# Optimization experiments

Measured on AMD Instinct MI355X. Metric: run time of the kernel, lower is better.

The kernel has to match this reference:

```python
import jax, jax.numpy as jnp
import numpy as np

L_LAYERS = 3
HIDDEN = 768
HEADS = 8
K_NEIGH = 5
LN_EPS = 1e-5


def layer_norm(x, scale, bias):
    mu = x.mean(-1, keepdims=True)
    var = ((x - mu) ** 2).mean(-1, keepdims=True)
    return (x - mu) * jax.lax.rsqrt(var + LN_EPS) * scale + bias


def build_adj_norm(x):
    """Dynamic kNN graph (topk on x x^T, symmetrized, dedup via boolean adjacency)
    with GCN self-loops and symmetric D^-1/2 A D^-1/2 normalization."""
    B, S, _ = x.shape
    sim = jnp.einsum('bsd,btd->bst', x, x)                     # [B,S,S]
    _, idx = jax.lax.top_k(sim, K_NEIGH)                        # [B,S,k]
    adj = jnp.zeros((B, S, S), dtype=bool)
    adj = adj.at[jnp.arange(B)[:, None, None],
                 jnp.arange(S)[None, :, None], idx].set(True)
    adj = adj | adj.transpose(0, 2, 1)                          # symmetrize (unique implied)
    adj = adj | jnp.eye(S, dtype=bool)[None]                    # remaining self-loops
    A = adj.astype(x.dtype)
    dinv = jax.lax.rsqrt(A.sum(-1))                             # deg>=1 always
    return dinv[:, :, None] * A * dinv[:, None, :]


def mha(x, w_in, b_in, w_out, b_out):
    B, S, D = x.shape
    d = D // HEADS
    qkv = x @ w_in + b_in                                       # [B,S,3D]
    q, k, v = jnp.split(qkv, 3, axis=-1)
    q = q.reshape(B, S, HEADS, d).transpose(0, 2, 1, 3)
    k = k.reshape(B, S, HEADS, d).transpose(0, 2, 1, 3)
    v = v.reshape(B, S, HEADS, d).transpose(0, 2, 1, 3)
    scores = jnp.einsum('bhqd,bhkd->bhqk', q, k) * (1.0 / np.sqrt(d))
    attn = jax.nn.softmax(scores, axis=-1)
    o = jnp.einsum('bhqk,bhkd->bhqd', attn, v)
    o = o.transpose(0, 2, 1, 3).reshape(B, S, D)
    return o @ w_out + b_out


def setup_inputs() -> dict:
    key = jax.random.key(0)
    ks = jax.random.split(key, 16)
    D, L = HIDDEN, L_LAYERS
    s = 0.02
    inp = {
        'x': jax.random.normal(ks[0], (8, 1024, D), dtype=jnp.float32),
        'gcn_w': jax.random.normal(ks[1], (L, D, D), dtype=jnp.float32) * s,
        'gcn_b': jnp.zeros((L, D), dtype=jnp.float32),
        'attn_in_w': jax.random.normal(ks[2], (L, D, 3 * D), dtype=jnp.float32) * s,
        'attn_in_b': jnp.zeros((L, 3 * D), dtype=jnp.float32),
        'attn_out_w': jax.random.normal(ks[3], (L, D, D), dtype=jnp.float32) * s,
        'attn_out_b': jnp.zeros((L, D), dtype=jnp.float32),
        'gate_w': jax.random.normal(ks[4], (L, 2 * D, D), dtype=jnp.float32) * s,
        'gate_b': jnp.zeros((L, D), dtype=jnp.float32),
        'ln_scale': jnp.ones((L, D), dtype=jnp.float32),
        'ln_bias': jnp.zeros((L, D), dtype=jnp.float32),
        'proj_w': jax.random.normal(ks[5], (D, D), dtype=jnp.float32) * s,
        'proj_b': jnp.zeros((D,), dtype=jnp.float32),
    }
    return inp


def reference(x, gcn_w, gcn_b, attn_in_w, attn_in_b, attn_out_w, attn_out_b,
              gate_w, gate_b, ln_scale, ln_bias, proj_w, proj_b):
    # Graph built once from the input embeddings (as in GCNTransformer.forward).
    A_norm = build_adj_norm(x)                                  # [B,S,S]
    h = x
    for l in range(L_LAYERS):
        gcn_out = jnp.einsum('bst,btd->bsd', A_norm, h @ gcn_w[l]) + gcn_b[l]
        attn_out = mha(h, attn_in_w[l], attn_in_b[l], attn_out_w[l], attn_out_b[l])
        gate = jax.nn.sigmoid(
            jnp.concatenate([gcn_out, attn_out], axis=-1) @ gate_w[l] + gate_b[l])
        fused = gate * gcn_out + (1.0 - gate) * attn_out
        h = layer_norm(fused + h, ln_scale[l], ln_bias[l])
    return h @ proj_w + proj_b
```

## Files before the change

kernel.cpp:

```cpp
#include <hip/hip_runtime.h>
#include <hip/hip_bf16.h>
#include <math.h>

using bf16 = __hip_bfloat16;
typedef short s16x8 __attribute__((ext_vector_type(8)));
typedef float f32x4 __attribute__((ext_vector_type(4)));

#define ROWS 8192
#define DH 768

static inline int cdiv(int a, int b) { return (a + b - 1) / b; }

__device__ __forceinline__ void gld16(const bf16* g, bf16* l)
{
    __builtin_amdgcn_global_load_lds(
        (const __attribute__((address_space(1))) void*)g,
        (__attribute__((address_space(3))) void*)l, 16, 0, 0);
}

__global__ __launch_bounds__(256)
void gemm_bf16_nt(const bf16* __restrict__ A, const bf16* __restrict__ Bt,
                  void* __restrict__ Cout, const float* __restrict__ bias,
                  int K, int lda, int ldb, int ldc,
                  long long aO, long long aI, long long bO, long long bI,
                  long long cO, long long cI, int zInner,
                  float scale, int storeBf16, int nMask)
{
    int z = blockIdx.z;
    int zo = z / zInner, zi = z - zo * zInner;
    const bf16* Ab = A + (long long)zo * aO + (long long)zi * aI;
    const bf16* Bb = Bt + (long long)zo * bO + (long long)zi * bI;
    long long cOff = (long long)zo * cO + (long long)zi * cI;

    __shared__ bf16 As[2 * 128 * 32];
    __shared__ bf16 Bs[2 * 128 * 32];

    int tid = threadIdx.x;
    int lane = tid & 63;
    int wid = tid >> 6;
    int wm = wid >> 1, wn = wid & 1;

    int nx = gridDim.x, ny = gridDim.y;
    int bx, by;
    if ((nx & 7) == 0) {
        int lin = blockIdx.y * nx + blockIdx.x;
        int t = lin >> 3;
        bx = (lin & 7) + (t / ny) * 8;
        by = t - (t / ny) * ny;
    } else { bx = blockIdx.x; by = blockIdx.y; }
    int m0 = bx * 128;
    int n0 = by * 128;

    f32x4 acc[4][4];
    f32x4 zero = {0.f, 0.f, 0.f, 0.f};
#pragma unroll
    for (int i = 0; i < 4; i++)
#pragma unroll
        for (int j = 0; j < 4; j++) acc[i][j] = zero;

    int f0 = tid, f1 = tid + 256;
    int r0 = f0 >> 2, c0 = (f0 & 3) * 8;
    int r1 = f1 >> 2, c1 = (f1 & 3) * 8;
    const bf16* a0p = Ab + (long long)(m0 + r0) * lda + c0;
    const bf16* a1p = Ab + (long long)(m0 + r1) * lda + c1;
    const bf16* b0p = Bb + (long long)(n0 + r0) * ldb + c0;
    const bf16* b1p = Bb + (long long)(n0 + r1) * ldb + c1;

    bf16* asw0 = As + wid * 512;
    bf16* asw1 = As + 2048 + wid * 512;
    bf16* bsw0 = Bs + wid * 512;
    bf16* bsw1 = Bs + 2048 + wid * 512;

    int mrow = lane & 15;
    int kcol = (lane >> 4) * 8;
    const bf16* aRead = As + (wm * 64 + mrow) * 32 + kcol;
    const bf16* bRead = Bs + (wn * 64 + mrow) * 32 + kcol;

    int nIter = K >> 5;
    gld16(a0p, asw0);
    gld16(a1p, asw1);
    gld16(b0p, bsw0);
    gld16(b1p, bsw1);

    for (int it = 0; it < nIter; it++) {
        __syncthreads();
        int cur = (it & 1) * 4096;
        int nxt = 4096 - cur;
        if (it + 1 < nIter) {
            int kn = (it + 1) << 5;
            gld16(a0p + kn, asw0 + nxt);
            gld16(a1p + kn, asw1 + nxt);
            gld16(b0p + kn, bsw0 + nxt);
            gld16(b1p + kn, bsw1 + nxt);
        }
        s16x8 af[4], bfr[4];
#pragma unroll
        for (int i = 0; i < 4; i++) af[i] = *(const s16x8*)(aRead + cur + i * 16 * 32);
#pragma unroll
        for (int i = 0; i < 4; i++) bfr[i] = *(const s16x8*)(bRead + cur + i * 16 * 32);
#pragma unroll
        for (int mi = 0; mi < 4; mi++)
#pragma unroll
            for (int ni = 0; ni < 4; ni++)
                acc[mi][ni] = __builtin_amdgcn_mfma_f32_16x16x32_bf16(
                    af[mi], bfr[ni], acc[mi][ni], 0, 0, 0);
    }

    int colL = lane & 15;
    int rq = (lane >> 4) * 4;
#pragma unroll
    for (int ni = 0; ni < 4; ni++) {
        int col = n0 + wn * 64 + ni * 16 + colL;
        if (col >= nMask) continue;
        float bv = bias ? bias[col] : 0.f;
#pragma unroll
        for (int mi = 0; mi < 4; mi++) {
#pragma unroll
            for (int r = 0; r < 4; r++) {
                int row = m0 + wm * 64 + mi * 16 + rq + r;
                float v = acc[mi][ni][r] * scale + bv;
                long long ci = cOff + (long long)row * ldc + col;
                if (storeBf16) ((bf16*)Cout)[ci] = __float2bfloat16(v);
                else           ((float*)Cout)[ci] = v;
            }
        }
    }
}

__global__ __launch_bounds__(256)
void flash_attn(const bf16* __restrict__ qkvb, const bf16* __restrict__ Vt,
                bf16* __restrict__ ob, float sscale)
{
    int qt = blockIdx.x, bh = blockIdx.y;
    int b = bh >> 3, h = bh & 7;
    int q0 = qt * 128;

    __shared__ bf16 Ks[128 * 96];
    __shared__ bf16 Ps[4 * 32 * 136];

    int tid = threadIdx.x, lane = tid & 63, wid = tid >> 6;
    int quad = lane >> 4, m16 = lane & 15;

    s16x8 qf[2][3];
#pragma unroll
    for (int s = 0; s < 2; s++) {
        int qrow = q0 + wid * 32 + s * 16 + m16;
        const bf16* qp = qkvb + (long long)(b * 1024 + qrow) * 2304 + h * 96 + quad * 8;
#pragma unroll
        for (int kk = 0; kk < 3; kk++)
            qf[s][kk] = *(const s16x8*)(qp + kk * 32);
    }

    f32x4 zero = {0.f, 0.f, 0.f, 0.f};
    f32x4 o_acc[2][6];
#pragma unroll
    for (int s = 0; s < 2; s++)
#pragma unroll
        for (int d = 0; d < 6; d++) o_acc[s][d] = zero;
    f32x4 m_run[2], l_run[2];
#pragma unroll
    for (int s = 0; s < 2; s++) {
        m_run[s] = {-3.0e38f, -3.0e38f, -3.0e38f, -3.0e38f};
        l_run[s] = zero;
    }

    bf16* Pw = Ps + wid * (32 * 136);
    const bf16* Kbase = qkvb + (long long)b * 1024 * 2304 + 768 + h * 96;
    const bf16* Vbase = Vt + (long long)bh * 128 * 1024;

    for (int kt = 0; kt < 8; kt++) {
        __syncthreads();
#pragma unroll
        for (int i = 0; i < 6; i++) {
            int gby = i * 4096 + wid * 1024 + lane * 16;
            int krow = gby / 192;
            int kcol = (gby - krow * 192) >> 1;
            gld16(Kbase + (long long)(kt * 128 + krow) * 2304 + kcol,
                  Ks + i * 2048 + wid * 512);
        }
        __syncthreads();

        f32x4 sacc[2][8];
#pragma unroll
        for (int s = 0; s < 2; s++)
#pragma unroll
            for (int j = 0; j < 8; j++) sacc[s][j] = zero;
#pragma unroll
        for (int j = 0; j < 8; j++) {
            s16x8 kf[3];
#pragma unroll
            for (int kk = 0; kk < 3; kk++)
                kf[kk] = *(const s16x8*)(Ks + (j * 16 + m16) * 96 + kk * 32 + quad * 8);
#pragma unroll
            for (int s = 0; s < 2; s++)
#pragma unroll
                for (int kk = 0; kk < 3; kk++)
                    sacc[s][j] = __builtin_amdgcn_mfma_f32_16x16x32_bf16(
                        qf[s][kk], kf[kk], sacc[s][j], 0, 0, 0);
        }

#pragma unroll
        for (int s = 0; s < 2; s++) {
#pragma unroll
            for (int j = 0; j < 8; j++)
#pragma unroll
                for (int c = 0; c < 4; c++) sacc[s][j][c] *= sscale;
            f32x4 tmax = sacc[s][0];
#pragma unroll
            for (int j = 1; j < 8; j++)
#pragma unroll
                for (int c = 0; c < 4; c++) tmax[c] = fmaxf(tmax[c], sacc[s][j][c]);
#pragma unroll
            for (int o = 1; o < 16; o <<= 1)
#pragma unroll
                for (int c = 0; c < 4; c++)
                    tmax[c] = fmaxf(tmax[c], __shfl_xor(tmax[c], o));
            f32x4 mnew, alpha;
#pragma unroll
            for (int c = 0; c < 4; c++) {
                mnew[c] = fmaxf(m_run[s][c], tmax[c]);
                alpha[c] = __expf(m_run[s][c] - mnew[c]);
            }
            f32x4 tsum = zero;
#pragma unroll
            for (int j = 0; j < 8; j++) {
#pragma unroll
                for (int c = 0; c < 4; c++) {
                    float pv = __expf(sacc[s][j][c] - mnew[c]);
                    tsum[c] += pv;
                    Pw[(s * 16 + quad * 4 + c) * 136 + j * 16 + m16] = __float2bfloat16(pv);
                }
            }
#pragma unroll
            for (int o = 1; o < 16; o <<= 1)
#pragma unroll
                for (int c = 0; c < 4; c++) tsum[c] += __shfl_xor(tsum[c], o);
#pragma unroll
            for (int c = 0; c < 4; c++)
                l_run[s][c] = l_run[s][c] * alpha[c] + tsum[c];
            m_run[s] = mnew;
#pragma unroll
            for (int d = 0; d < 6; d++)
#pragma unroll
                for (int c = 0; c < 4; c++) o_acc[s][d][c] *= alpha[c];
        }

        s16x8 pf[2][4];
#pragma unroll
        for (int s = 0; s < 2; s++)
#pragma unroll
            for (int kk = 0; kk < 4; kk++)
                pf[s][kk] = *(const s16x8*)(Pw + (s * 16 + m16) * 136 + kk * 32 + quad * 8);
#pragma unroll
        for (int dt = 0; dt < 6; dt++) {
            s16x8 vf[4];
#pragma unroll
            for (int kk = 0; kk < 4; kk++)
                vf[kk] = *(const s16x8*)(Vbase + (long long)(dt * 16 + m16) * 1024
                                         + kt * 128 + kk * 32 + quad * 8);
#pragma unroll
            for (int s = 0; s < 2; s++)
#pragma unroll
                for (int kk = 0; kk < 4; kk++)
                    o_acc[s][dt] = __builtin_amdgcn_mfma_f32_16x16x32_bf16(
                        pf[s][kk], vf[kk], o_acc[s][dt], 0, 0, 0);
        }
    }

#pragma unroll
    for (int s = 0; s < 2; s++) {
        f32x4 inv;
#pragma unroll
        for (int c = 0; c < 4; c++) inv[c] = 1.f / l_run[s][c];
#pragma unroll
        for (int dt = 0; dt < 6; dt++) {
#pragma unroll
            for (int c = 0; c < 4; c++) {
                int row = q0 + wid * 32 + s * 16 + quad * 4 + c;
                int col = h * 96 + dt * 16 + m16;
                ob[(long long)(b * 1024 + row) * 768 + col] =
                    __float2bfloat16(o_acc[s][dt][c] * inv[c]);
            }
        }
    }
}

__global__ __launch_bounds__(256)
void transpose_cast(const float* __restrict__ in, bf16* __restrict__ out, int K, int N)
{
    long long zoff = (long long)blockIdx.z * K * N;
    int k0 = blockIdx.x * 32, n0 = blockIdx.y * 32;
    __shared__ float t[32][33];
    int tx = threadIdx.x & 31, ty = threadIdx.x >> 5;
#pragma unroll
    for (int j = 0; j < 32; j += 8)
        t[ty + j][tx] = in[zoff + (long long)(k0 + ty + j) * N + n0 + tx];
    __syncthreads();
#pragma unroll
    for (int j = 0; j < 32; j += 8)
        out[zoff + (long long)(n0 + ty + j) * K + k0 + tx] = __float2bfloat16(t[tx][ty + j]);
}

__global__ void zero_u64(unsigned long long* __restrict__ p, int n)
{
    int i = blockIdx.x * 256 + threadIdx.x;
    if (i < n) p[i] = 0ull;
}

__global__ __launch_bounds__(256)
void prep_x(const float* __restrict__ x, float* __restrict__ h,
            bf16* __restrict__ hb, bf16* __restrict__ xc)
{
    int i = blockIdx.x * 256 + threadIdx.x;
    if (i >= ROWS * DH) return;
    float v = x[i];
    h[i] = v;
    bf16 h1 = __float2bfloat16(v);
    float r1 = v - __bfloat162float(h1);
    bf16 h2 = __float2bfloat16(r1);
    hb[i] = h1;
    int row = i / DH, d = i - row * DH;
    long long xb = (long long)row * 3072;
    xc[xb + d] = h1;
    xc[xb + 768 + d] = h1;
    xc[xb + 1536 + d] = h2;
    xc[xb + 2304 + d] = h1;
}

__global__ __launch_bounds__(256)
void topk_rerank(const float* __restrict__ sim, const float* __restrict__ x,
                 unsigned long long* __restrict__ mask)
{
    int row = blockIdx.x;
    int b = row >> 10, s = row & 1023;
    int tid = threadIdx.x;
    int wid = tid >> 6, lane = tid & 63;

    __shared__ float wvals[4][8];
    __shared__ int   widx[4][8];
    __shared__ int   cand[8];
    __shared__ double val[8];

    int base = wid * 256 + lane * 4;
    float4 vv = *(const float4*)(sim + (long long)row * 1024 + base);
    float v0 = vv.x, v1 = vv.y, v2 = vv.z, v3 = vv.w;

    for (int r = 0; r < 8; r++) {
        float bv = v0; int bi = base;
        if (v1 > bv) { bv = v1; bi = base + 1; }
        if (v2 > bv) { bv = v2; bi = base + 2; }
        if (v3 > bv) { bv = v3; bi = base + 3; }
#pragma unroll
        for (int o = 1; o < 64; o <<= 1) {
            float ov = __shfl_xor(bv, o);
            int   oi = __shfl_xor(bi, o);
            if (ov > bv || (ov == bv && oi < bi)) { bv = ov; bi = oi; }
        }
        if ((bi >> 2) == (wid * 64 + lane)) {
            int sl = bi & 3;
            if (sl == 0) v0 = -3.4e38f;
            else if (sl == 1) v1 = -3.4e38f;
            else if (sl == 2) v2 = -3.4e38f;
            else v3 = -3.4e38f;
        }
        if (lane == 0) { wvals[wid][r] = bv; widx[wid][r] = bi; }
    }
    __syncthreads();
    if (wid == 0) {
        float mv = -3.4e38f; int mi = 0x7fffffff;
        if (lane < 32) { mv = wvals[lane >> 3][lane & 7]; mi = widx[lane >> 3][lane & 7]; }
        for (int r = 0; r < 8; r++) {
            float bv = mv; int bi = mi;
#pragma unroll
            for (int o = 1; o < 32; o <<= 1) {
                float ov = __shfl_xor(bv, o, 32);
                int   oi = __shfl_xor(bi, o, 32);
                if (ov > bv || (ov == bv && oi < bi)) { bv = ov; bi = oi; }
            }
            if (lane < 32 && bi == mi) mv = -3.4e38f;
            if (lane == 0) cand[r] = bi;
        }
    }
    __syncthreads();
    int g = tid >> 5, t = tid & 31;
    int c = cand[g];
    const float4* xs4 = (const float4*)(x + (long long)row * DH);
    const float4* xc4 = (const float4*)(x + ((long long)b * 1024 + c) * DH);
    double acc = 0.0;
#pragma unroll
    for (int j = 0; j < 6; j++) {
        float4 a = xs4[t + j * 32];
        float4 q = xc4[t + j * 32];
        acc += (double)a.x * q.x + (double)a.y * q.y
             + (double)a.z * q.z + (double)a.w * q.w;
    }
#pragma unroll
    for (int o = 16; o; o >>= 1) acc += __shfl_xor(acc, o, 32);
    if (t == 0) val[g] = acc;
    __syncthreads();
    if (tid == 0) {
        bool used[8] = {false, false, false, false, false, false, false, false};
        for (int r = 0; r < 5; r++) {
            int best = -1;
            for (int j = 0; j < 8; j++) {
                if (used[j]) continue;
                if (best < 0 || val[j] > val[best] ||
                    (val[j] == val[best] && cand[j] < cand[best])) best = j;
            }
            used[best] = true;
            int ci = cand[best];
            atomicOr(&mask[((long long)b * 1024 + s) * 16 + (ci >> 6)], 1ull << (ci & 63));
            atomicOr(&mask[((long long)b * 1024 + ci) * 16 + (s >> 6)], 1ull << (s & 63));
        }
        atomicOr(&mask[(long long)row * 16 + (s >> 6)], 1ull << (s & 63));
    }
}

__global__ void calc_dinv(const unsigned long long* __restrict__ mask,
                          float* __restrict__ dinv, int n)
{
    int i = blockIdx.x * 256 + threadIdx.x;
    if (i >= n) return;
    int c = 0;
#pragma unroll
    for (int w = 0; w < 16; w++) c += __popcll(mask[(long long)i * 16 + w]);
    dinv[i] = 1.f / sqrtf((float)c);
}

__global__ __launch_bounds__(256)
void spmm(const unsigned long long* __restrict__ mask, const float* __restrict__ dinv,
          const float* __restrict__ g, const float* __restrict__ bias,
          float* __restrict__ out)
{
    int s = blockIdx.x, b = blockIdx.y;
    int row = b * 1024 + s;
    __shared__ unsigned long long mrow[16];
    int tid = threadIdx.x;
    if (tid < 16) mrow[tid] = mask[(long long)row * 16 + tid];
    __syncthreads();
    float ds = dinv[row];
    float a0 = 0.f, a1 = 0.f, a2 = 0.f;
    const float* gb = g + (long long)b * 1024 * DH;
    const float* db = dinv + b * 1024;
    for (int w = 0; w < 16; w++) {
        unsigned long long bits = mrow[w];
        while (bits) {
            int t = (w << 6) + __ffsll(bits) - 1;
            bits &= bits - 1;
            float c = ds * db[t];
            const float* gr = gb + (long long)t * DH;
            a0 += c * gr[tid];
            a1 += c * gr[tid + 256];
            a2 += c * gr[tid + 512];
        }
    }
    float* o = out + (long long)row * DH;
    o[tid] = a0 + bias[tid];
    o[tid + 256] = a1 + bias[tid + 256];
    o[tid + 512] = a2 + bias[tid + 512];
}

__global__ __launch_bounds__(256)
void vt_transpose(const bf16* __restrict__ qkvb, bf16* __restrict__ Vt)
{
    int bh = blockIdx.y;
    int b = bh >> 3, h = bh & 7;
    int t0 = blockIdx.x * 64;
    __shared__ bf16 tile[64][100];
    int tid = threadIdx.x;
    {
        int t = tid >> 2, c0 = (tid & 3) * 24;
        const bf16* src = qkvb + ((long long)(b * 1024 + t0 + t)) * 2304 + 1536 + h * 96 + c0;
#pragma unroll
        for (int j = 0; j < 24; j++) tile[t][c0 + j] = src[j];
    }
    __syncthreads();
    bf16* dst = Vt + ((long long)bh * 128) * 1024 + t0;
    bf16 zb = __float2bfloat16(0.f);
#pragma unroll
    for (int j = 0; j < 32; j++) {
        int f = tid + j * 256;
        int d = f >> 6, t = f & 63;
        dst[(long long)d * 1024 + t] = (d < 96) ? tile[t][d] : zb;
    }
}

__global__ void concat_cast(const float* __restrict__ gcn_out, const float* __restrict__ attn_out,
                            bf16* __restrict__ gi)
{
    int i = blockIdx.x * 256 + threadIdx.x;
    if (i >= ROWS * DH) return;
    int r = i / DH, d = i - r * DH;
    gi[(long long)r * 1536 + d] = __float2bfloat16(gcn_out[i]);
    gi[(long long)r * 1536 + 768 + d] = __float2bfloat16(attn_out[i]);
}

__global__ __launch_bounds__(256)
void fuse_ln(const float* __restrict__ gate_lin, const float* __restrict__ gcn_out,
             const float* __restrict__ attn_out, float* __restrict__ h, bf16* __restrict__ hb,
             const float* __restrict__ lns, const float* __restrict__ lnb)
{
    int row = blockIdx.x;
    long long base = (long long)row * DH;
    int tid = threadIdx.x;
    __shared__ float red[4];
    float xv[3];
#pragma unroll
    for (int j = 0; j < 3; j++) {
        int d = tid + j * 256;
        float gl = gate_lin[base + d];
        float gv = 1.f / (1.f + __expf(-gl));
        float f = gv * gcn_out[base + d] + (1.f - gv) * attn_out[base + d];
        xv[j] = f + h[base + d];
    }
    float s = xv[0] + xv[1] + xv[2];
    for (int o = 32; o; o >>= 1) s += __shfl_xor(s, o);
    if ((tid & 63) == 0) red[tid >> 6] = s;
    __syncthreads();
    float mu = (red[0] + red[1] + red[2] + red[3]) * (1.f / 768.f);
    __syncthreads();
    float vs = 0.f;
#pragma unroll
    for (int j = 0; j < 3; j++) { float c = xv[j] - mu; vs += c * c; }
    for (int o = 32; o; o >>= 1) vs += __shfl_xor(vs, o);
    if ((tid & 63) == 0) red[tid >> 6] = vs;
    __syncthreads();
    float var = (red[0] + red[1] + red[2] + red[3]) * (1.f / 768.f);
    float rs = 1.f / sqrtf(var + 1e-5f);
#pragma unroll
    for (int j = 0; j < 3; j++) {
        int d = tid + j * 256;
        float y = (xv[j] - mu) * rs * lns[d] + lnb[d];
        h[base + d] = y;
        hb[base + d] = __float2bfloat16(y);
    }
}

static void gemm(hipStream_t st, const bf16* A, const bf16* Bt, void* C, const float* bias,
                 int M, int N, int K, int lda, int ldb, int ldc,
                 long long aO, long long aI, long long bO, long long bI,
                 long long cO, long long cI, int zInner, int Z,
                 float scale, int storeBf16, int nMask)
{
    dim3 g(M / 128, (N + 127) / 128, Z);
    gemm_bf16_nt<<<g, dim3(256), 0, st>>>(A, Bt, C, bias, K, lda, ldb, ldc,
                                          aO, aI, bO, bI, cO, cI, zInner,
                                          scale, storeBf16, nMask);
}

extern "C" void kernel_launch(void* const* d_in, const int* in_sizes, int n_in,
                              void* d_out, int out_size, void* d_ws, size_t ws_size,
                              hipStream_t stream)
{
    (void)in_sizes; (void)n_in; (void)out_size; (void)ws_size;
    const float* x      = (const float*)d_in[0];
    const float* gcn_w  = (const float*)d_in[1];
    const float* gcn_b  = (const float*)d_in[2];
    const float* ain_w  = (const float*)d_in[3];
    const float* ain_b  = (const float*)d_in[4];
    const float* aout_w = (const float*)d_in[5];
    const float* aout_b = (const float*)d_in[6];
    const float* gate_w = (const float*)d_in[7];
    const float* gate_b = (const float*)d_in[8];
    const float* ln_s   = (const float*)d_in[9];
    const float* ln_b   = (const float*)d_in[10];
    const float* proj_w = (const float*)d_in[11];
    const float* proj_b = (const float*)d_in[12];
    float* out = (float*)d_out;

    char* p = (char*)d_ws;
    auto alloc = [&](size_t bytes) {
        char* r = p;
        p += (bytes + 255) & ~(size_t)255;
        return r;
    };
    bf16* gcn_wt  = (bf16*)alloc((size_t)3 * 768 * 768 * 2);
    bf16* ain_wt  = (bf16*)alloc((size_t)3 * 2304 * 768 * 2);
    bf16* aout_wt = (bf16*)alloc((size_t)3 * 768 * 768 * 2);
    bf16* gate_wt = (bf16*)alloc((size_t)3 * 768 * 1536 * 2);
    bf16* proj_wt = (bf16*)alloc((size_t)768 * 768 * 2);
    bf16* hb      = (bf16*)alloc((size_t)ROWS * DH * 2);
    float* h      = (float*)alloc((size_t)ROWS * DH * 4);
    bf16* qkvb    = (bf16*)alloc((size_t)ROWS * 2304 * 2);
    bf16* gateinb = qkvb;
    float* sim    = (float*)alloc((size_t)ROWS * 1024 * 4);
    float* attn_o = sim;
    unsigned long long* mask = (unsigned long long*)alloc((size_t)ROWS * 16 * 8);
    float* dinv   = (float*)alloc((size_t)ROWS * 4);
    float* g      = (float*)alloc((size_t)ROWS * DH * 4);
    float* gate_l = g;
    float* gcn_o  = (float*)alloc((size_t)ROWS * DH * 4);
    bf16* Vt      = (bf16*)alloc((size_t)64 * 128 * 1024 * 2);
    bf16* ob      = (bf16*)alloc((size_t)ROWS * DH * 2);
    bf16* xc      = (bf16*)g;

    transpose_cast<<<dim3(24, 24, 3), 256, 0, stream>>>(gcn_w, gcn_wt, 768, 768);
    transpose_cast<<<dim3(24, 72, 3), 256, 0, stream>>>(ain_w, ain_wt, 768, 2304);
    transpose_cast<<<dim3(24, 24, 3), 256, 0, stream>>>(aout_w, aout_wt, 768, 768);
    transpose_cast<<<dim3(48, 24, 3), 256, 0, stream>>>(gate_w, gate_wt, 1536, 768);
    transpose_cast<<<dim3(24, 24, 1), 256, 0, stream>>>(proj_w, proj_wt, 768, 768);

    prep_x<<<cdiv(ROWS * DH, 256), 256, 0, stream>>>(x, h, hb, xc);

    gemm(stream, xc, xc + 768, sim, nullptr, 1024, 1024, 2304, 3072, 3072, 1024,
         (long long)1024 * 3072, 0, (long long)1024 * 3072, 0,
         (long long)1024 * 1024, 0, 1, 8, 1.f, 0, 1024);

    zero_u64<<<cdiv(ROWS * 16, 256), 256, 0, stream>>>(mask, ROWS * 16);
    topk_rerank<<<ROWS, 256, 0, stream>>>(sim, x, mask);
    calc_dinv<<<cdiv(ROWS, 256), 256, 0, stream>>>(mask, dinv, ROWS);

    float sscale = 1.0f / sqrtf(96.0f);

    for (int l = 0; l < 3; l++) {
        gemm(stream, hb, gcn_wt + (long long)l * 768 * 768, g, nullptr,
             ROWS, 768, 768, 768, 768, 768, 0, 0, 0, 0, 0, 0, 1, 1, 1.f, 0, 768);
        spmm<<<dim3(1024, 8), 256, 0, stream>>>(mask, dinv, g, gcn_b + l * 768, gcn_o);
        gemm(stream, hb, ain_wt + (long long)l * 2304 * 768, qkvb, ain_b + l * 2304,
             ROWS, 2304, 768, 768, 768, 2304, 0, 0, 0, 0, 0, 0, 1, 1, 1.f, 1, 2304);
        vt_transpose<<<dim3(16, 64), 256, 0, stream>>>(qkvb, Vt);
        flash_attn<<<dim3(8, 64), 256, 0, stream>>>(qkvb, Vt, ob, sscale);
        gemm(stream, ob, aout_wt + (long long)l * 768 * 768, attn_o, aout_b + l * 768,
             ROWS, 768, 768, 768, 768, 768, 0, 0, 0, 0, 0, 0, 1, 1, 1.f, 0, 768);
        concat_cast<<<cdiv(ROWS * DH, 256), 256, 0, stream>>>(gcn_o, attn_o, gateinb);
        gemm(stream, gateinb, gate_wt + (long long)l * 768 * 1536, gate_l, gate_b + l * 768,
             ROWS, 768, 1536, 1536, 1536, 768, 0, 0, 0, 0, 0, 0, 1, 1, 1.f, 0, 768);
        fuse_ln<<<ROWS, 256, 0, stream>>>(gate_l, gcn_o, attn_o, h, hb,
                                          ln_s + l * 768, ln_b + l * 768);
    }

    gemm(stream, hb, proj_wt, out, proj_b,
         ROWS, 768, 768, 768, 768, 768, 0, 0, 0, 0, 0, 0, 1, 1, 1.f, 0, 768);
}
```

Before: 1.166 ms.

## Fuse GCN and QKV projections, write bf16 gate input directly, simplify sim GEMM

Concatenates the GCN weight into the QKV projection so one GEMM with N=3072 produces q, k, v and the GCN features in bf16. The spmm and output-projection GEMM now write bf16 straight into the gate-input buffer, which removes concat_cast and the fp32 intermediates. The similarity GEMM drops the split-bf16 compensated K=2304 trick and runs plain bf16 with K=768. Flash attention switches to exp2 with a log2e-folded scale and a swapped grid order. Lower precision for the GCN features and the similarity scores could change top-k neighbour selection and overall accuracy.

```diff
diff --git a/kernel.cpp b/kernel.cpp
--- a/kernel.cpp
+++ b/kernel.cpp
@@ -24,7 +24,7 @@
                   int K, int lda, int ldb, int ldc,
                   long long aO, long long aI, long long bO, long long bI,
                   long long cO, long long cI, int zInner,
-                  float scale, int storeBf16, int nMask)
+                  float scale, int storeBf16, int nMask, int biasN)
 {
     int z = blockIdx.z;
     int zo = z / zInner, zi = z - zo * zInner;
@@ -112,7 +112,7 @@
     for (int ni = 0; ni < 4; ni++) {
         int col = n0 + wn * 64 + ni * 16 + colL;
         if (col >= nMask) continue;
-        float bv = bias ? bias[col] : 0.f;
+        float bv = (bias && col < biasN) ? bias[col] : 0.f;
 #pragma unroll
         for (int mi = 0; mi < 4; mi++) {
 #pragma unroll
@@ -128,10 +128,10 @@
 }
 
 __global__ __launch_bounds__(256)
-void flash_attn(const bf16* __restrict__ qkvb, const bf16* __restrict__ Vt,
-                bf16* __restrict__ ob, float sscale)
-{
-    int qt = blockIdx.x, bh = blockIdx.y;
+void flash_attn(const bf16* __restrict__ qg, const bf16* __restrict__ Vt,
+                bf16* __restrict__ ob, float cs)
+{
+    int bh = blockIdx.x, qt = blockIdx.y;
     int b = bh >> 3, h = bh & 7;
     int q0 = qt * 128;
 
@@ -145,7 +145,7 @@
 #pragma unroll
     for (int s = 0; s < 2; s++) {
         int qrow = q0 + wid * 32 + s * 16 + m16;
-        const bf16* qp = qkvb + (long long)(b * 1024 + qrow) * 2304 + h * 96 + quad * 8;
+        const bf16* qp = qg + (long long)(b * 1024 + qrow) * 3072 + h * 96 + quad * 8;
 #pragma unroll
         for (int kk = 0; kk < 3; kk++)
             qf[s][kk] = *(const s16x8*)(qp + kk * 32);
@@ -165,7 +165,7 @@
     }
 
     bf16* Pw = Ps + wid * (32 * 136);
-    const bf16* Kbase = qkvb + (long long)b * 1024 * 2304 + 768 + h * 96;
+    const bf16* Kbase = qg + (long long)b * 1024 * 3072 + 768 + h * 96;
     const bf16* Vbase = Vt + (long long)bh * 128 * 1024;
 
     for (int kt = 0; kt < 8; kt++) {
@@ -175,7 +175,7 @@
             int gby = i * 4096 + wid * 1024 + lane * 16;
             int krow = gby / 192;
             int kcol = (gby - krow * 192) >> 1;
-            gld16(Kbase + (long long)(kt * 128 + krow) * 2304 + kcol,
+            gld16(Kbase + (long long)(kt * 128 + krow) * 3072 + kcol,
                   Ks + i * 2048 + wid * 512);
         }
         __syncthreads();
@@ -204,7 +204,7 @@
 #pragma unroll
             for (int j = 0; j < 8; j++)
 #pragma unroll
-                for (int c = 0; c < 4; c++) sacc[s][j][c] *= sscale;
+                for (int c = 0; c < 4; c++) sacc[s][j][c] *= cs;
             f32x4 tmax = sacc[s][0];
 #pragma unroll
             for (int j = 1; j < 8; j++)
@@ -219,14 +219,14 @@
 #pragma unroll
             for (int c = 0; c < 4; c++) {
                 mnew[c] = fmaxf(m_run[s][c], tmax[c]);
-                alpha[c] = __expf(m_run[s][c] - mnew[c]);
+                alpha[c] = exp2f(m_run[s][c] - mnew[c]);
             }
             f32x4 tsum = zero;
 #pragma unroll
             for (int j = 0; j < 8; j++) {
 #pragma unroll
                 for (int c = 0; c < 4; c++) {
-                    float pv = __expf(sacc[s][j][c] - mnew[c]);
+                    float pv = exp2f(sacc[s][j][c] - mnew[c]);
                     tsum[c] += pv;
                     Pw[(s * 16 + quad * 4 + c) * 136 + j * 16 + m16] = __float2bfloat16(pv);
                 }
@@ -286,19 +286,21 @@
 }
 
 __global__ __launch_bounds__(256)
-void transpose_cast(const float* __restrict__ in, bf16* __restrict__ out, int K, int N)
-{
-    long long zoff = (long long)blockIdx.z * K * N;
+void transpose_cast(const float* __restrict__ in, bf16* __restrict__ out,
+                    int K, int N, long long inZ, long long outZ)
+{
+    long long izoff = (long long)blockIdx.z * inZ;
+    long long ozoff = (long long)blockIdx.z * outZ;
     int k0 = blockIdx.x * 32, n0 = blockIdx.y * 32;
     __shared__ float t[32][33];
     int tx = threadIdx.x & 31, ty = threadIdx.x >> 5;
 #pragma unroll
     for (int j = 0; j < 32; j += 8)
-        t[ty + j][tx] = in[zoff + (long long)(k0 + ty + j) * N + n0 + tx];
+        t[ty + j][tx] = in[izoff + (long long)(k0 + ty + j) * N + n0 + tx];
     __syncthreads();
 #pragma unroll
     for (int j = 0; j < 32; j += 8)
-        out[zoff + (long long)(n0 + ty + j) * K + k0 + tx] = __float2bfloat16(t[tx][ty + j]);
+        out[ozoff + (long long)(n0 + ty + j) * K + k0 + tx] = __float2bfloat16(t[tx][ty + j]);
 }
 
 __global__ void zero_u64(unsigned long long* __restrict__ p, int n)
@@ -309,22 +311,13 @@
 
 __global__ __launch_bounds__(256)
 void prep_x(const float* __restrict__ x, float* __restrict__ h,
-            bf16* __restrict__ hb, bf16* __restrict__ xc)
+            bf16* __restrict__ hb)
 {
     int i = blockIdx.x * 256 + threadIdx.x;
     if (i >= ROWS * DH) return;
     float v = x[i];
     h[i] = v;
-    bf16 h1 = __float2bfloat16(v);
-    float r1 = v - __bfloat162float(h1);
-    bf16 h2 = __float2bfloat16(r1);
-    hb[i] = h1;
-    int row = i / DH, d = i - row * DH;
-    long long xb = (long long)row * 3072;
-    xc[xb + d] = h1;
-    xc[xb + 768 + d] = h1;
-    xc[xb + 1536 + d] = h2;
-    xc[xb + 2304 + d] = h1;
+    hb[i] = __float2bfloat16(v);
 }
 
 __global__ __launch_bounds__(256)
@@ -429,8 +422,8 @@
 
 __global__ __launch_bounds__(256)
 void spmm(const unsigned long long* __restrict__ mask, const float* __restrict__ dinv,
-          const float* __restrict__ g, const float* __restrict__ bias,
-          float* __restrict__ out)
+          const bf16* __restrict__ qg, const float* __restrict__ bias,
+          bf16* __restrict__ gout)
 {
     int s = blockIdx.x, b = blockIdx.y;
     int row = b * 1024 + s;
@@ -440,7 +433,7 @@
     __syncthreads();
     float ds = dinv[row];
     float a0 = 0.f, a1 = 0.f, a2 = 0.f;
-    const float* gb = g + (long long)b * 1024 * DH;
+    const bf16* gb = qg + (long long)b * 1024 * 3072 + 2304;
     const float* db = dinv + b * 1024;
     for (int w = 0; w < 16; w++) {
         unsigned long long bits = mrow[w];
@@ -448,20 +441,20 @@
             int t = (w << 6) + __ffsll(bits) - 1;
             bits &= bits - 1;
             float c = ds * db[t];
-            const float* gr = gb + (long long)t * DH;
-            a0 += c * gr[tid];
-            a1 += c * gr[tid + 256];
-            a2 += c * gr[tid + 512];
-        }
-    }
-    float* o = out + (long long)row * DH;
-    o[tid] = a0 + bias[tid];
-    o[tid + 256] = a1 + bias[tid + 256];
-    o[tid + 512] = a2 + bias[tid + 512];
-}
-
-__global__ __launch_bounds__(256)
-void vt_transpose(const bf16* __restrict__ qkvb, bf16* __restrict__ Vt)
+            const bf16* gr = gb + (long long)t * 3072;
+            a0 += c * __bfloat162float(gr[tid]);
+            a1 += c * __bfloat162float(gr[tid + 256]);
+            a2 += c * __bfloat162float(gr[tid + 512]);
+        }
+    }
+    bf16* o = gout + (long long)row * 1536;
+    o[tid]       = __float2bfloat16(a0 + bias[tid]);
+    o[tid + 256] = __float2bfloat16(a1 + bias[tid + 256]);
+    o[tid + 512] = __float2bfloat16(a2 + bias[tid + 512]);
+}
+
+__global__ __launch_bounds__(256)
+void vt_transpose(const bf16* __restrict__ qg, bf16* __restrict__ Vt)
 {
     int bh = blockIdx.y;
     int b = bh >> 3, h = bh & 7;
@@ -470,7 +463,7 @@
     int tid = threadIdx.x;
     {
         int t = tid >> 2, c0 = (tid & 3) * 24;
-        const bf16* src = qkvb + ((long long)(b * 1024 + t0 + t)) * 2304 + 1536 + h * 96 + c0;
+        const bf16* src = qg + ((long long)(b * 1024 + t0 + t)) * 3072 + 1536 + h * 96 + c0;
 #pragma unroll
         for (int j = 0; j < 24; j++) tile[t][c0 + j] = src[j];
     }
@@ -485,23 +478,14 @@
     }
 }
 
-__global__ void concat_cast(const float* __restrict__ gcn_out, const float* __restrict__ attn_out,
-                            bf16* __restrict__ gi)
-{
-    int i = blockIdx.x * 256 + threadIdx.x;
-    if (i >= ROWS * DH) return;
-    int r = i / DH, d = i - r * DH;
-    gi[(long long)r * 1536 + d] = __float2bfloat16(gcn_out[i]);
-    gi[(long long)r * 1536 + 768 + d] = __float2bfloat16(attn_out[i]);
-}
-
-__global__ __launch_bounds__(256)
-void fuse_ln(const float* __restrict__ gate_lin, const float* __restrict__ gcn_out,
-             const float* __restrict__ attn_out, float* __restrict__ h, bf16* __restrict__ hb,
+__global__ __launch_bounds__(256)
+void fuse_ln(const float* __restrict__ gate_lin, const bf16* __restrict__ gi,
+             float* __restrict__ h, bf16* __restrict__ hb,
              const float* __restrict__ lns, const float* __restrict__ lnb)
 {
     int row = blockIdx.x;
     long long base = (long long)row * DH;
+    long long gbase = (long long)row * 1536;
     int tid = threadIdx.x;
     __shared__ float red[4];
     float xv[3];
@@ -510,7 +494,9 @@
         int d = tid + j * 256;
         float gl = gate_lin[base + d];
         float gv = 1.f / (1.f + __expf(-gl));
-        float f = gv * gcn_out[base + d] + (1.f - gv) * attn_out[base + d];
+        float gcn = __bfloat162float(gi[gbase + d]);
+        float attn = __bfloat162float(gi[gbase + 768 + d]);
+        float f = gv * gcn + (1.f - gv) * attn;
         xv[j] = f + h[base + d];
     }
     float s = xv[0] + xv[1] + xv[2];
@@ -540,12 +526,12 @@
                  int M, int N, int K, int lda, int ldb, int ldc,
                  long long aO, long long aI, long long bO, long long bI,
                  long long cO, long long cI, int zInner, int Z,
-                 float scale, int storeBf16, int nMask)
+                 float scale, int storeBf16, int nMask, int biasN)
 {
     dim3 g(M / 128, (N + 127) / 128, Z);
     gemm_bf16_nt<<<g, dim3(256), 0, st>>>(A, Bt, C, bias, K, lda, ldb, ldc,
                                           aO, aI, bO, bI, cO, cI, zInner,
-                                          scale, storeBf16, nMask);
+                                          scale, storeBf16, nMask, biasN);
 }
 
 extern "C" void kernel_launch(void* const* d_in, const int* in_sizes, int n_in,
@@ -574,61 +560,63 @@
         p += (bytes + 255) & ~(size_t)255;
         return r;
     };
-    bf16* gcn_wt  = (bf16*)alloc((size_t)3 * 768 * 768 * 2);
-    bf16* ain_wt  = (bf16*)alloc((size_t)3 * 2304 * 768 * 2);
+    bf16* qgw     = (bf16*)alloc((size_t)3 * 3072 * 768 * 2);
     bf16* aout_wt = (bf16*)alloc((size_t)3 * 768 * 768 * 2);
     bf16* gate_wt = (bf16*)alloc((size_t)3 * 768 * 1536 * 2);
     bf16* proj_wt = (bf16*)alloc((size_t)768 * 768 * 2);
     bf16* hb      = (bf16*)alloc((size_t)ROWS * DH * 2);
     float* h      = (float*)alloc((size_t)ROWS * DH * 4);
-    bf16* qkvb    = (bf16*)alloc((size_t)ROWS * 2304 * 2);
-    bf16* gateinb = qkvb;
+    bf16* qg      = (bf16*)alloc((size_t)ROWS * 3072 * 2);
     float* sim    = (float*)alloc((size_t)ROWS * 1024 * 4);
-    float* attn_o = sim;
+    bf16* Vt      = (bf16*)sim;
     unsigned long long* mask = (unsigned long long*)alloc((size_t)ROWS * 16 * 8);
     float* dinv   = (float*)alloc((size_t)ROWS * 4);
-    float* g      = (float*)alloc((size_t)ROWS * DH * 4);
-    float* gate_l = g;
-    float* gcn_o  = (float*)alloc((size_t)ROWS * DH * 4);
-    bf16* Vt      = (bf16*)alloc((size_t)64 * 128 * 1024 * 2);
+    float* gate_l = (float*)alloc((size_t)ROWS * DH * 4);
+    bf16* gateinb = (bf16*)alloc((size_t)ROWS * 1536 * 2);
     bf16* ob      = (bf16*)alloc((size_t)ROWS * DH * 2);
-    bf16* xc      = (bf16*)g;
-
-    transpose_cast<<<dim3(24, 24, 3), 256, 0, stream>>>(gcn_w, gcn_wt, 768, 768);
-    transpose_cast<<<dim3(24, 72, 3), 256, 0, stream>>>(ain_w, ain_wt, 768, 2304);
-    transpose_cast<<<dim3(24, 24, 3), 256, 0, stream>>>(aout_w, aout_wt, 768, 768);
-    transpose_cast<<<dim3(48, 24, 3), 256, 0, stream>>>(gate_w, gate_wt, 1536, 768);
-    transpose_cast<<<dim3(24, 24, 1), 256, 0, stream>>>(proj_w, proj_wt, 768, 768);
-
-    prep_x<<<cdiv(ROWS * DH, 256), 256, 0, stream>>>(x, h, hb, xc);
-
-    gemm(stream, xc, xc + 768, sim, nullptr, 1024, 1024, 2304, 3072, 3072, 1024,
-         (long long)1024 * 3072, 0, (long long)1024 * 3072, 0,
-         (long long)1024 * 1024, 0, 1, 8, 1.f, 0, 1024);
+
+    transpose_cast<<<dim3(24, 72, 3), 256, 0, stream>>>(
+        ain_w, qgw, 768, 2304, (long long)768 * 2304, (long long)3072 * 768);
+    transpose_cast<<<dim3(24, 24, 3), 256, 0, stream>>>(
+        gcn_w, qgw + (long long)2304 * 768, 768, 768,
+        (long long)768 * 768, (long long)3072 * 768);
+    transpose_cast<<<dim3(24, 24, 3), 256, 0, stream>>>(
+        aout_w, aout_wt, 768, 768, (long long)768 * 768, (long long)768 * 768);
+    transpose_cast<<<dim3(48, 24, 3), 256, 0, stream>>>(
+        gate_w, gate_wt, 1536, 768, (long long)1536 * 768, (long long)768 * 1536);
+    transpose_cast<<<dim3(24, 24, 1), 256, 0, stream>>>(
+        proj_w, proj_wt, 768, 768, 0, 0);
+
+    prep_x<<<cdiv(ROWS * DH, 256), 256, 0, stream>>>(x, h, hb);
+
+    gemm(stream, hb, hb, sim, nullptr, 1024, 1024, 768, 768, 768, 1024,
+         (long long)1024 * 768, 0, (long long)1024 * 768, 0,
+         (long long)1024 * 1024, 0, 1, 8, 1.f, 0, 1024, 0);
 
     zero_u64<<<cdiv(ROWS * 16, 256), 256, 0, stream>>>(mask, ROWS * 16);
     topk_rerank<<<ROWS, 256, 0, stream>>>(sim, x, mask);
     calc_dinv<<<cdiv(ROWS, 256), 256, 0, stream>>>(mask, dinv, ROWS);
 
-    float sscale = 1.0f / sqrtf(96.0f);
+    float cs = 1.4426950408889634f / sqrtf(96.0f);
 
     for (int l = 0; l < 3; l++) {
-        gemm(stream, hb, gcn_wt + (long long)l * 768 * 768, g, nullptr,
-             ROWS, 768, 768, 768, 768, 768, 0, 0, 0, 0, 0, 0, 1, 1, 1.f, 0, 768);
-        spmm<<<dim3(1024, 8), 256, 0, stream>>>(mask, dinv, g, gcn_b + l * 768, gcn_o);
-        gemm(stream, hb, ain_wt + (long long)l * 2304 * 768, qkvb, ain_b + l * 2304,
-             ROWS, 2304, 768, 768, 768, 2304, 0, 0, 0, 0, 0, 0, 1, 1, 1.f, 1, 2304);
-        vt_transpose<<<dim3(16, 64), 256, 0, stream>>>(qkvb, Vt);
-        flash_attn<<<dim3(8, 64), 256, 0, stream>>>(qkvb, Vt, ob, sscale);
-        gemm(stream, ob, aout_wt + (long long)l * 768 * 768, attn_o, aout_b + l * 768,
-             ROWS, 768, 768, 768, 768, 768, 0, 0, 0, 0, 0, 0, 1, 1, 1.f, 0, 768);
-        concat_cast<<<cdiv(ROWS * DH, 256), 256, 0, stream>>>(gcn_o, attn_o, gateinb);
-        gemm(stream, gateinb, gate_wt + (long long)l * 768 * 1536, gate_l, gate_b + l * 768,
-             ROWS, 768, 1536, 1536, 1536, 768, 0, 0, 0, 0, 0, 0, 1, 1, 1.f, 0, 768);
-        fuse_ln<<<ROWS, 256, 0, stream>>>(gate_l, gcn_o, attn_o, h, hb,
+        gemm(stream, hb, qgw + (long long)l * 3072 * 768, qg, ain_b + l * 2304,
+             ROWS, 3072, 768, 768, 768, 3072, 0, 0, 0, 0, 0, 0, 1, 1,
+             1.f, 1, 3072, 2304);
+        spmm<<<dim3(1024, 8), 256, 0, stream>>>(mask, dinv, qg, gcn_b + l * 768, gateinb);
+        vt_transpose<<<dim3(16, 64), 256, 0, stream>>>(qg, Vt);
+        flash_attn<<<dim3(64, 8), 256, 0, stream>>>(qg, Vt, ob, cs);
+        gemm(stream, ob, aout_wt + (long long)l * 768 * 768,
+             (void*)(gateinb + 768), aout_b + l * 768,
+             ROWS, 768, 768, 768, 768, 1536, 0, 0, 0, 0, 0, 0, 1, 1,
+             1.f, 1, 768, 768);
+        gemm(stream, gateinb, gate_wt + (long long)l * 768 * 1536, gate_l,
+             gate_b + l * 768, ROWS, 768, 1536, 1536, 1536, 768,
+             0, 0, 0, 0, 0, 0, 1, 1, 1.f, 0, 768, 768);
+        fuse_ln<<<ROWS, 256, 0, stream>>>(gate_l, gateinb, h, hb,
                                           ln_s + l * 768, ln_b + l * 768);
     }
 
     gemm(stream, hb, proj_wt, out, proj_b,
-         ROWS, 768, 768, 768, 768, 768, 0, 0, 0, 0, 0, 0, 1, 1, 1.f, 0, 768);
-}
+         ROWS, 768, 768, 768, 768, 768, 0, 0, 0, 0, 0, 0, 1, 1, 1.f, 0, 768, 768);
+}
```

After: 1.012 ms. 1.15x faster.
